# Kernel tuning notes

Hardware: AMD Instinct MI355X
Metric: run time of the kernel (lower is better)

Reference implementation:

```python
import jax, jax.numpy as jnp
import numpy as np

N_NODES = 100000
N_EDGES = 3200000
NEG_SLOPE = 0.2  # PyG GATConv default


def _gat_conv(x, src, dst, W, a_src, a_dst, b, num_nodes):
    # x: [N, Fin]; src/dst: [E'] (self-loops already appended)
    h = x @ W                                   # [N, Fout]
    alpha_src = h @ a_src                       # [N]
    alpha_dst = h @ a_dst                       # [N]
    e = jax.nn.leaky_relu(alpha_src[src] + alpha_dst[dst], NEG_SLOPE)  # [E']
    # segment softmax over incoming edges of each destination node
    e_max = jax.ops.segment_max(e, dst, num_segments=num_nodes)
    e_exp = jnp.exp(e - e_max[dst])
    denom = jax.ops.segment_sum(e_exp, dst, num_segments=num_nodes)
    alpha = e_exp / (denom[dst] + 1e-16)        # [E']
    out = jax.ops.segment_sum(h[src] * alpha[:, None], dst, num_segments=num_nodes)
    return out + b


def setup_inputs() -> dict:
    key = jax.random.key(0)
    ks = jax.random.split(key, 10)
    x = jax.random.normal(ks[0], (N_NODES, 1), jnp.float32)
    edge_index = jax.random.randint(ks[1], (2, N_EDGES), 0, N_NODES, dtype=jnp.int64)
    s1 = 1.0  # glorot-ish scales
    return {
        "x": x,
        "edge_index": edge_index,
        "W1": jax.random.normal(ks[2], (1, 20), jnp.float32) * s1,
        "a_src1": jax.random.normal(ks[3], (20,), jnp.float32) * 0.3,
        "a_dst1": jax.random.normal(ks[4], (20,), jnp.float32) * 0.3,
        "b1": jnp.zeros((20,), jnp.float32),
        "W2": jax.random.normal(ks[5], (20, 20), jnp.float32) * (1.0 / np.sqrt(20.0)),
        "a_src2": jax.random.normal(ks[6], (20,), jnp.float32) * 0.3,
        "a_dst2": jax.random.normal(ks[7], (20,), jnp.float32) * 0.3,
        "b2": jnp.zeros((20,), jnp.float32),
        "Wl": jax.random.normal(ks[8], (20, 1), jnp.float32) * (1.0 / np.sqrt(20.0)),
        "bl": jnp.zeros((1,), jnp.float32),
    }


def reference(x, edge_index, W1, a_src1, a_dst1, b1, W2, a_src2, a_dst2, b2, Wl, bl):
    n = x.shape[0]
    loop = jnp.arange(n, dtype=edge_index.dtype)
    src = jnp.concatenate([edge_index[0], loop])  # add_self_loops=True
    dst = jnp.concatenate([edge_index[1], loop])
    h = _gat_conv(x, src, dst, W1, a_src1, a_dst1, b1, n)
    h = jax.nn.relu(h)
    h = _gat_conv(h, src, dst, W2, a_src2, a_dst2, b2, n)
    h = jax.nn.relu(h)
    return h @ Wl + bl  # [N, 1]
```

## Files before the change

kernel.cpp:

```cpp
#include <hip/hip_runtime.h>
#include <hip/hip_fp16.h>

#define FDIM 20
#define NSLOPE 0.2f
#define BSHIFT 7
#define BSIZE 128
#define BCAP 4800
#define MAXBUCK 800
#define PGRID 256
#define HSTRIDE 32
#define ABLK 512

__device__ __forceinline__ float lrelu(float v) { return v > 0.f ? v : NSLOPE * v; }

__global__ void k_init(const float* __restrict__ x, const float* __restrict__ W1,
                       const float* __restrict__ a_src, const float* __restrict__ a_dst,
                       float2* __restrict__ PX, float* __restrict__ AD,
                       int* __restrict__ gcur, int N)
{
    int i = blockIdx.x * blockDim.x + threadIdx.x;
    if (i < MAXBUCK) gcur[i] = 0;
    if (i >= N) return;
    float cs = 0.f, cd = 0.f;
#pragma unroll
    for (int f = 0; f < FDIM; ++f) { float w = W1[f]; cs += w * a_src[f]; cd += w * a_dst[f]; }
    float xv = x[i];
    PX[i] = make_float2(xv * cs, xv);
    AD[i] = xv * cd;
}

__global__ void __launch_bounds__(1024)
k_part(const int* __restrict__ ei, int E, int nbuck,
       int* __restrict__ gcur, int* __restrict__ slab)
{
    __shared__ int hist[MAXBUCK];
    __shared__ int base[MAXBUCK];
    const int chunk = (E + PGRID - 1) / PGRID;
    const int c0 = blockIdx.x * chunk;
    const int c1 = min(c0 + chunk, E);
    for (int t = threadIdx.x; t < nbuck; t += 1024) hist[t] = 0;
    __syncthreads();
    int i = c0 + 2 * threadIdx.x;
    for (; i + 1 < c1; i += 2048) {
        int2 d2 = *(const int2*)(ei + E + i);
        atomicAdd(&hist[d2.x >> BSHIFT], 1);
        atomicAdd(&hist[d2.y >> BSHIFT], 1);
    }
    if (i < c1) atomicAdd(&hist[ei[E + i] >> BSHIFT], 1);
    __syncthreads();
    for (int t = threadIdx.x; t < nbuck; t += 1024) {
        int c = hist[t];
        base[t] = c ? atomicAdd(gcur + t, c) : 0;
        hist[t] = 0;
    }
    __syncthreads();
    i = c0 + 2 * threadIdx.x;
    for (; i + 1 < c1; i += 2048) {
        int2 s2 = *(const int2*)(ei + i);
        int2 d2 = *(const int2*)(ei + E + i);
        int bA = d2.x >> BSHIFT, bB = d2.y >> BSHIFT;
        int lpA = atomicAdd(&hist[bA], 1);
        int lpB = atomicAdd(&hist[bB], 1);
        int pA = base[bA] + lpA;
        int pB = base[bB] + lpB;
        if (pA < BCAP) slab[(size_t)bA * BCAP + pA] = (s2.x << BSHIFT) | (d2.x & (BSIZE - 1));
        if (pB < BCAP) slab[(size_t)bB * BCAP + pB] = (s2.y << BSHIFT) | (d2.y & (BSIZE - 1));
    }
    if (i < c1) {
        int s = ei[i], d = ei[E + i];
        int b = d >> BSHIFT;
        int lp = atomicAdd(&hist[b], 1);
        int pos = base[b] + lp;
        if (pos < BCAP) slab[(size_t)b * BCAP + pos] = (s << BSHIFT) | (d & (BSIZE - 1));
    }
}

__device__ __forceinline__ void sort_bucket(const int* __restrict__ sp, int cnt,
                                            int* __restrict__ sedge,
                                            int* __restrict__ off,
                                            int* __restrict__ cur)
{
    const int tid = threadIdx.x;
    if (tid < BSIZE + 1) off[tid] = 0;
    __syncthreads();
    for (int i = tid; i < cnt; i += blockDim.x)
        atomicAdd(&off[(sp[i] & (BSIZE - 1)) + 1], 1);
    __syncthreads();
    for (int o = 1; o < BSIZE; o <<= 1) {
        int v = 0;
        if (tid < BSIZE && tid + 1 > o) v = off[tid + 1 - o];
        __syncthreads();
        if (tid < BSIZE) off[tid + 1] += v;
        __syncthreads();
    }
    if (tid < BSIZE) cur[tid] = off[tid];
    __syncthreads();
    for (int i = tid; i < cnt; i += blockDim.x) {
        int e = sp[i];
        int pos = atomicAdd(&cur[e & (BSIZE - 1)], 1);
        sedge[pos] = e >> BSHIFT;
    }
    __syncthreads();
}

__global__ void __launch_bounds__(ABLK)
k_agg1(const int* __restrict__ gcur, const int* __restrict__ slab,
       const float2* __restrict__ PX, const float* __restrict__ AD,
       const float* __restrict__ W1, const float* __restrict__ b1,
       const float* __restrict__ W2,
       const float* __restrict__ as2w, const float* __restrict__ ad2w,
       __half* __restrict__ H, float* __restrict__ AD2, int N)
{
    __shared__ int sedge[BCAP];
    __shared__ int off[BSIZE + 1], cur[BSIZE];
    __shared__ float sAD[BSIZE];
    __shared__ float sW1[FDIM], sb1[FDIM], sW2[FDIM * FDIM], sas[FDIM], sad[FDIM];
    const int tid = threadIdx.x;
    const int b = blockIdx.x;
    const int dbase = b << BSHIFT;
    if (tid < BSIZE) { int d = dbase + tid; sAD[tid] = (d < N) ? AD[d] : 0.f; }
    for (int t = tid; t < FDIM * FDIM; t += ABLK) sW2[t] = W2[t];
    if (tid >= 480 && tid < 480 + FDIM) {
        int k = tid - 480;
        sW1[k] = W1[k]; sb1[k] = b1[k]; sas[k] = as2w[k]; sad[k] = ad2w[k];
    }
    const int cnt = min(gcur[b], BCAP);
    sort_bucket(slab + (size_t)b * BCAP, cnt, sedge, off, cur);

    const int dl = tid >> 2, sub = tid & 3;
    const float adv = sAD[dl];
    float den = 0.f, sx = 0.f;
    const int e1 = off[dl + 1];
#pragma unroll 2
    for (int j = off[dl] + sub; j < e1; j += 4) {
        int s = sedge[j];
        float2 p = PX[s];
        float w = __expf(lrelu(p.x + adv));
        den += w; sx += w * p.y;
    }
    den += __shfl_xor(den, 1); den += __shfl_xor(den, 2);
    sx  += __shfl_xor(sx, 1);  sx  += __shfl_xor(sx, 2);
    const int d = dbase + dl;
    if (sub == 0 && d < N) {
        float2 p = PX[d];
        float w = __expf(lrelu(p.x + adv));
        den += w; sx += w * p.y;
        float sv = sx / (den + 1e-16f);
        float tk[FDIM];
#pragma unroll
        for (int k = 0; k < FDIM; ++k) {
            float tv = sv * sW1[k] + sb1[k];
            tk[k] = tv > 0.f ? tv : 0.f;
        }
        float pas = 0.f, pad = 0.f;
        __half2* hrow = (__half2*)(H + (size_t)d * HSTRIDE);
#pragma unroll
        for (int f = 0; f < FDIM; f += 2) {
            float h0 = 0.f, h1 = 0.f;
#pragma unroll
            for (int k = 0; k < FDIM; ++k) {
                h0 += tk[k] * sW2[k * FDIM + f];
                h1 += tk[k] * sW2[k * FDIM + f + 1];
            }
            hrow[f >> 1] = __halves2half2(__float2half(h0), __float2half(h1));
            pas += h0 * sas[f] + h1 * sas[f + 1];
            pad += h0 * sad[f] + h1 * sad[f + 1];
        }
        *(float*)(H + (size_t)d * HSTRIDE + FDIM) = pas;
        AD2[d] = pad;
    }
}

__global__ void __launch_bounds__(ABLK)
k_agg2(const int* __restrict__ gcur, const int* __restrict__ slab,
       const __half* __restrict__ H, const float* __restrict__ AD2,
       const float* __restrict__ b2, const float* __restrict__ Wl,
       const float* __restrict__ bl,
       float* __restrict__ out, int N)
{
    __shared__ int sedge[BCAP];
    __shared__ int off[BSIZE + 1], cur[BSIZE];
    __shared__ float sAD[BSIZE];
    __shared__ float sb2[FDIM], sWl[FDIM];
    const int tid = threadIdx.x;
    const int b = blockIdx.x;
    const int dbase = b << BSHIFT;
    if (tid < BSIZE) { int d = dbase + tid; sAD[tid] = (d < N) ? AD2[d] : 0.f; }
    if (tid >= 480 && tid < 480 + FDIM) {
        int k = tid - 480;
        sb2[k] = b2[k]; sWl[k] = Wl[k];
    }
    const int cnt = min(gcur[b], BCAP);
    sort_bucket(slab + (size_t)b * BCAP, cnt, sedge, off, cur);

    const int dl = tid >> 2, sub = tid & 3;
    const float adv = sAD[dl];
    float den = 0.f;
    float acc[FDIM];
#pragma unroll
    for (int k = 0; k < FDIM; ++k) acc[k] = 0.f;
    const int e1 = off[dl + 1];
#pragma unroll 2
    for (int j = off[dl] + sub; j < e1; j += 4) {
        int s = sedge[j];
        const uint4* rp = (const uint4*)(H + (size_t)s * HSTRIDE);
        uint4 a = rp[0];
        uint4 bb = rp[1];
        uint4 c = rp[2];
        float w = __expf(lrelu(__uint_as_float(c.z) + adv));
        den += w;
        float2 f;
        f = __half22float2(*(__half2*)&a.x);  acc[0]  += w * f.x; acc[1]  += w * f.y;
        f = __half22float2(*(__half2*)&a.y);  acc[2]  += w * f.x; acc[3]  += w * f.y;
        f = __half22float2(*(__half2*)&a.z);  acc[4]  += w * f.x; acc[5]  += w * f.y;
        f = __half22float2(*(__half2*)&a.w);  acc[6]  += w * f.x; acc[7]  += w * f.y;
        f = __half22float2(*(__half2*)&bb.x); acc[8]  += w * f.x; acc[9]  += w * f.y;
        f = __half22float2(*(__half2*)&bb.y); acc[10] += w * f.x; acc[11] += w * f.y;
        f = __half22float2(*(__half2*)&bb.z); acc[12] += w * f.x; acc[13] += w * f.y;
        f = __half22float2(*(__half2*)&bb.w); acc[14] += w * f.x; acc[15] += w * f.y;
        f = __half22float2(*(__half2*)&c.x);  acc[16] += w * f.x; acc[17] += w * f.y;
        f = __half22float2(*(__half2*)&c.y);  acc[18] += w * f.x; acc[19] += w * f.y;
    }
    den += __shfl_xor(den, 1); den += __shfl_xor(den, 2);
#pragma unroll
    for (int k = 0; k < FDIM; ++k) {
        acc[k] += __shfl_xor(acc[k], 1);
        acc[k] += __shfl_xor(acc[k], 2);
    }
    const int d = dbase + dl;
    if (sub == 0 && d < N) {
        const uint4* rp = (const uint4*)(H + (size_t)d * HSTRIDE);
        uint4 a = rp[0], bb = rp[1], c = rp[2];
        float w = __expf(lrelu(__uint_as_float(c.z) + adv));
        den += w;
        float hv[FDIM];
        float2 f;
        f = __half22float2(*(__half2*)&a.x);  hv[0]  = f.x; hv[1]  = f.y;
        f = __half22float2(*(__half2*)&a.y);  hv[2]  = f.x; hv[3]  = f.y;
        f = __half22float2(*(__half2*)&a.z);  hv[4]  = f.x; hv[5]  = f.y;
        f = __half22float2(*(__half2*)&a.w);  hv[6]  = f.x; hv[7]  = f.y;
        f = __half22float2(*(__half2*)&bb.x); hv[8]  = f.x; hv[9]  = f.y;
        f = __half22float2(*(__half2*)&bb.y); hv[10] = f.x; hv[11] = f.y;
        f = __half22float2(*(__half2*)&bb.z); hv[12] = f.x; hv[13] = f.y;
        f = __half22float2(*(__half2*)&bb.w); hv[14] = f.x; hv[15] = f.y;
        f = __half22float2(*(__half2*)&c.x);  hv[16] = f.x; hv[17] = f.y;
        f = __half22float2(*(__half2*)&c.y);  hv[18] = f.x; hv[19] = f.y;
        float inv = 1.f / (den + 1e-16f);
        float r = 0.f;
#pragma unroll
        for (int k = 0; k < FDIM; ++k) {
            float v = (acc[k] + w * hv[k]) * inv + sb2[k];
            v = v > 0.f ? v : 0.f;
            r += v * sWl[k];
        }
        out[d] = r + bl[0];
    }
}

extern "C" void kernel_launch(void* const* d_in, const int* in_sizes, int n_in,
                              void* d_out, int out_size, void* d_ws, size_t ws_size,
                              hipStream_t stream)
{
    const float* x      = (const float*)d_in[0];
    const int*   ei     = (const int*)d_in[1];
    const float* W1     = (const float*)d_in[2];
    const float* a_src1 = (const float*)d_in[3];
    const float* a_dst1 = (const float*)d_in[4];
    const float* b1     = (const float*)d_in[5];
    const float* W2     = (const float*)d_in[6];
    const float* a_src2 = (const float*)d_in[7];
    const float* a_dst2 = (const float*)d_in[8];
    const float* b2     = (const float*)d_in[9];
    const float* Wl     = (const float*)d_in[10];
    const float* bl     = (const float*)d_in[11];
    float* out = (float*)d_out;

    const int N = in_sizes[0];
    const int E = in_sizes[1] / 2;
    const int NBUCK = (N + BSIZE - 1) >> BSHIFT;

    __half* H   = (__half*)d_ws;
    float2* PX  = (float2*)(H + (size_t)N * HSTRIDE);
    float*  AD  = (float*)(PX + N);
    float*  AD2 = AD + N;
    int*  gcur  = (int*)(AD2 + N);
    int*  slab  = gcur + MAXBUCK;

    const int nb_n = (N + 255) / 256;

    k_init<<<nb_n, 256, 0, stream>>>(x, W1, a_src1, a_dst1, PX, AD, gcur, N);
    k_part<<<PGRID, 1024, 0, stream>>>(ei, E, NBUCK, gcur, slab);
    k_agg1<<<NBUCK, ABLK, 0, stream>>>(gcur, slab, PX, AD, W1, b1, W2,
                                       a_src2, a_dst2, H, AD2, N);
    k_agg2<<<NBUCK, ABLK, 0, stream>>>(gcur, slab, H, AD2, b2, Wl, bl, out, N);
}
```

Measured before the change: 195.3 us.

## Reuse sorted per-bucket edge list from layer one in layer two aggregation

The first aggregation kernel now writes its locally sorted edge list and CSR offsets to global memory, and the second aggregation kernel reads them directly instead of re-sorting the bucket slab in shared memory. The partition kernel also rounds each block's slot reservation up to a multiple of 16 and fills the padding with -1 sentinels, which the sort skips, and the slab capacity is raised to absorb the padding. This removes the duplicate counting sort and its barriers in the second layer. In exchange it adds global writes in layer one, uncached global reads of edge indices in layer two, a larger slab, and padding-fill writes whose purpose (write alignment) is unclear.

```diff
diff --git a/kernel.cpp b/kernel.cpp
--- a/kernel.cpp
+++ b/kernel.cpp
@@ -5,7 +5,8 @@
 #define NSLOPE 0.2f
 #define BSHIFT 7
 #define BSIZE 128
-#define BCAP 4800
+#define BCAP 7168
+#define SCAP 4800
 #define MAXBUCK 800
 #define PGRID 256
 #define HSTRIDE 32
@@ -50,7 +51,8 @@
     __syncthreads();
     for (int t = threadIdx.x; t < nbuck; t += 1024) {
         int c = hist[t];
-        base[t] = c ? atomicAdd(gcur + t, c) : 0;
+        int r = (c + 15) & ~15;
+        base[t] = r ? atomicAdd(gcur + t, r) : 0;
         hist[t] = 0;
     }
     __syncthreads();
@@ -73,34 +75,16 @@
         int pos = base[b] + lp;
         if (pos < BCAP) slab[(size_t)b * BCAP + pos] = (s << BSHIFT) | (d & (BSIZE - 1));
     }
-}
-
-__device__ __forceinline__ void sort_bucket(const int* __restrict__ sp, int cnt,
-                                            int* __restrict__ sedge,
-                                            int* __restrict__ off,
-                                            int* __restrict__ cur)
-{
-    const int tid = threadIdx.x;
-    if (tid < BSIZE + 1) off[tid] = 0;
-    __syncthreads();
-    for (int i = tid; i < cnt; i += blockDim.x)
-        atomicAdd(&off[(sp[i] & (BSIZE - 1)) + 1], 1);
-    __syncthreads();
-    for (int o = 1; o < BSIZE; o <<= 1) {
-        int v = 0;
-        if (tid < BSIZE && tid + 1 > o) v = off[tid + 1 - o];
-        __syncthreads();
-        if (tid < BSIZE) off[tid + 1] += v;
-        __syncthreads();
-    }
-    if (tid < BSIZE) cur[tid] = off[tid];
-    __syncthreads();
-    for (int i = tid; i < cnt; i += blockDim.x) {
-        int e = sp[i];
-        int pos = atomicAdd(&cur[e & (BSIZE - 1)], 1);
-        sedge[pos] = e >> BSHIFT;
-    }
-    __syncthreads();
+    __syncthreads();
+    for (int t = threadIdx.x; t < nbuck; t += 1024) {
+        int c = hist[t];
+        int r = (c + 15) & ~15;
+        int b0 = base[t];
+        for (int j = c; j < r; ++j) {
+            int pos = b0 + j;
+            if (pos < BCAP) slab[(size_t)t * BCAP + pos] = -1;
+        }
+    }
 }
 
 __global__ void __launch_bounds__(ABLK)
@@ -109,9 +93,10 @@
        const float* __restrict__ W1, const float* __restrict__ b1,
        const float* __restrict__ W2,
        const float* __restrict__ as2w, const float* __restrict__ ad2w,
-       __half* __restrict__ H, float* __restrict__ AD2, int N)
-{
-    __shared__ int sedge[BCAP];
+       __half* __restrict__ H, float* __restrict__ AD2,
+       int* __restrict__ gsedge, int* __restrict__ goff, int N)
+{
+    __shared__ int sedge[SCAP];
     __shared__ int off[BSIZE + 1], cur[BSIZE];
     __shared__ float sAD[BSIZE];
     __shared__ float sW1[FDIM], sb1[FDIM], sW2[FDIM * FDIM], sas[FDIM], sad[FDIM];
@@ -124,8 +109,37 @@
         int k = tid - 480;
         sW1[k] = W1[k]; sb1[k] = b1[k]; sas[k] = as2w[k]; sad[k] = ad2w[k];
     }
+    if (tid < BSIZE + 1) off[tid] = 0;
+    __syncthreads();
+
     const int cnt = min(gcur[b], BCAP);
-    sort_bucket(slab + (size_t)b * BCAP, cnt, sedge, off, cur);
+    const int* sp = slab + (size_t)b * BCAP;
+    for (int i = tid; i < cnt; i += ABLK) {
+        int e = sp[i];
+        if (e >= 0) atomicAdd(&off[(e & (BSIZE - 1)) + 1], 1);
+    }
+    __syncthreads();
+    for (int o = 1; o < BSIZE; o <<= 1) {
+        int v = 0;
+        if (tid < BSIZE && tid + 1 > o) v = off[tid + 1 - o];
+        __syncthreads();
+        if (tid < BSIZE) off[tid + 1] += v;
+        __syncthreads();
+    }
+    if (tid < BSIZE) cur[tid] = off[tid];
+    __syncthreads();
+    for (int i = tid; i < cnt; i += ABLK) {
+        int e = sp[i];
+        if (e >= 0) {
+            int pos = atomicAdd(&cur[e & (BSIZE - 1)], 1);
+            sedge[pos] = e >> BSHIFT;
+        }
+    }
+    __syncthreads();
+
+    const int cntT = off[BSIZE];
+    for (int i = tid; i < cntT; i += ABLK) gsedge[(size_t)b * SCAP + i] = sedge[i];
+    if (tid < BSIZE + 1) goff[b * (BSIZE + 1) + tid] = off[tid];
 
     const int dl = tid >> 2, sub = tid & 3;
     const float adv = sAD[dl];
@@ -172,27 +186,27 @@
 }
 
 __global__ void __launch_bounds__(ABLK)
-k_agg2(const int* __restrict__ gcur, const int* __restrict__ slab,
+k_agg2(const int* __restrict__ gsedge, const int* __restrict__ goff,
        const __half* __restrict__ H, const float* __restrict__ AD2,
        const float* __restrict__ b2, const float* __restrict__ Wl,
        const float* __restrict__ bl,
        float* __restrict__ out, int N)
 {
-    __shared__ int sedge[BCAP];
-    __shared__ int off[BSIZE + 1], cur[BSIZE];
+    __shared__ int off[BSIZE + 1];
     __shared__ float sAD[BSIZE];
     __shared__ float sb2[FDIM], sWl[FDIM];
     const int tid = threadIdx.x;
     const int b = blockIdx.x;
     const int dbase = b << BSHIFT;
     if (tid < BSIZE) { int d = dbase + tid; sAD[tid] = (d < N) ? AD2[d] : 0.f; }
+    if (tid < BSIZE + 1) off[tid] = goff[b * (BSIZE + 1) + tid];
     if (tid >= 480 && tid < 480 + FDIM) {
         int k = tid - 480;
         sb2[k] = b2[k]; sWl[k] = Wl[k];
     }
-    const int cnt = min(gcur[b], BCAP);
-    sort_bucket(slab + (size_t)b * BCAP, cnt, sedge, off, cur);
-
+    __syncthreads();
+
+    const int* sl = gsedge + (size_t)b * SCAP;
     const int dl = tid >> 2, sub = tid & 3;
     const float adv = sAD[dl];
     float den = 0.f;
@@ -202,7 +216,7 @@
     const int e1 = off[dl + 1];
 #pragma unroll 2
     for (int j = off[dl] + sub; j < e1; j += 4) {
-        int s = sedge[j];
+        int s = sl[j];
         const uint4* rp = (const uint4*)(H + (size_t)s * HSTRIDE);
         uint4 a = rp[0];
         uint4 bb = rp[1];
@@ -279,18 +293,20 @@
     const int E = in_sizes[1] / 2;
     const int NBUCK = (N + BSIZE - 1) >> BSHIFT;
 
-    __half* H   = (__half*)d_ws;
-    float2* PX  = (float2*)(H + (size_t)N * HSTRIDE);
-    float*  AD  = (float*)(PX + N);
-    float*  AD2 = AD + N;
-    int*  gcur  = (int*)(AD2 + N);
-    int*  slab  = gcur + MAXBUCK;
+    __half* H    = (__half*)d_ws;
+    float2* PX   = (float2*)(H + (size_t)N * HSTRIDE);
+    float*  AD   = (float*)(PX + N);
+    float*  AD2  = AD + N;
+    int*  gcur   = (int*)(AD2 + N);
+    int*  goff   = gcur + MAXBUCK;
+    int*  slab   = goff + MAXBUCK * (BSIZE + 1);
+    int*  gsedge = slab + (size_t)MAXBUCK * BCAP;
 
     const int nb_n = (N + 255) / 256;
 
     k_init<<<nb_n, 256, 0, stream>>>(x, W1, a_src1, a_dst1, PX, AD, gcur, N);
     k_part<<<PGRID, 1024, 0, stream>>>(ei, E, NBUCK, gcur, slab);
     k_agg1<<<NBUCK, ABLK, 0, stream>>>(gcur, slab, PX, AD, W1, b1, W2,
-                                       a_src2, a_dst2, H, AD2, N);
-    k_agg2<<<NBUCK, ABLK, 0, stream>>>(gcur, slab, H, AD2, b2, Wl, bl, out, N);
-}
+                                       a_src2, a_dst2, H, AD2, gsedge, goff, N);
+    k_agg2<<<NBUCK, ABLK, 0, stream>>>(gsedge, goff, H, AD2, b2, Wl, bl, out, N);
+}
```

New measurement: 218.9 us. 1.12x slower.
